# Performance work log

Hardware: AMD Instinct MI355X
Metric: run time of the kernel (lower is better)

Reference implementation:

```python
import jax, jax.numpy as jnp
import numpy as np
from jax import lax

STD_H, STD_W = 364, 280
RADIUS, SIGMA = 15, 4.0


def gaussian_kernel():
    r = jnp.arange(-RADIUS, RADIUS + 1, dtype=jnp.float32)
    d2 = r[:, None] ** 2 + r[None, :] ** 2
    k = jnp.exp(-0.5 / (SIGMA ** 2) * d2)
    k = k / k.sum()
    return k[None, None]  # (1,1,31,31) OIHW


def setup_inputs() -> dict:
    key = jax.random.key(0)
    k1, k2 = jax.random.split(key)
    B, H, W = 32, 512, 512
    input_face = jax.random.uniform(k1, (B, 3, H, W), dtype=jnp.float32)
    # landmarks in (x, y) pixel coords within the HxW image
    landmarks = jax.random.uniform(k2, (B, 68, 2), dtype=jnp.float32) * jnp.array([W, H], jnp.float32)
    weight = gaussian_kernel()
    return {"input_face": input_face, "landmarks": landmarks, "weight": weight}


def _blur(x, weight):
    # x: (B,1,h,w), 31x31 'same' conv (kernel symmetric, so corr == conv)
    return lax.conv_general_dilated(x, weight, (1, 1), 'SAME',
                                    dimension_numbers=('NCHW', 'OIHW', 'NCHW'))


def reference(input_face, landmarks, weight):
    B, C, H, W = input_face.shape
    scaling = STD_H / H
    lm = landmarks * scaling                      # (B,68,2) in standard coords
    center = lm[:, 30:31, :]                      # (B,1,2)

    p0 = lm[:, 30:36, :]
    p1 = lm[:, 2:15, :]
    p2 = lm[:, 48:68, :]
    p3 = lm[:, 6:11, :]
    p01 = (p0 - center) * 1.5 + center
    p11 = (p1 - center) * 0.5 + center
    p12 = (p1 - center) * 0.7 + center
    p13 = (p1 - center) * 0.9 + center
    p21 = (p2 - center) * 1.3 + center
    keys = jnp.concatenate([p0, p01, p12, p13, p11, p2, p3, p21], axis=-2)  # (B,96,2)

    iy = jnp.round(jnp.clip(keys[..., 1], 0, STD_H - 1)).astype(jnp.int32)
    ix = jnp.round(jnp.clip(keys[..., 0], 0, STD_W - 1)).astype(jnp.int32)

    # Faithful to torch advanced-indexing semantics: union of ALL batches'
    # points is written into every batch's heatmap.
    hm = jnp.zeros((STD_H, STD_W), jnp.float32).at[iy.ravel(), ix.ravel()].set(1.0)
    hm = jnp.broadcast_to(hm[None, None], (B, 1, STD_H, STD_W))

    w1 = _blur(hm, weight)
    w2 = jnp.where(w1 > 1e-7, 1.0, w1)
    w3 = _blur(w2, weight)

    w_mask = jax.image.resize(w3, (B, 1, H, W), method='bilinear')
    return (1.0 - w_mask) * input_face  # filling='black'
```

## Files before the change

### kernel.cpp

```cpp
#include <hip/hip_runtime.h>

#define BB   32
#define HH   512
#define WW   512
#define SH   364
#define SW   280
#define RAD  15
#define NK   96
#define OMN  (HH*WW)
#define PF4  (OMN/4)

#define OH   16
#define OW   32
#define NRM  13
#define NCM  19
#define WRM  (NRM + 2*RAD)
#define HRM  (NRM + 4*RAD)
#define HCP  84
#define WCP  52
#define NCP  20
#define G1   13
#define G2   5

typedef float f4 __attribute__((ext_vector_type(4)));

__device__ __forceinline__ void point_ij(const float* __restrict__ lm, int b, int j,
                                         int& ix, int& iy) {
    int idx; float s;
    if      (j <  6) { idx = 30 + j;        s = 1.0f; }
    else if (j < 12) { idx = 30 + (j - 6);  s = 1.5f; }
    else if (j < 25) { idx =  2 + (j - 12); s = 0.7f; }
    else if (j < 38) { idx =  2 + (j - 25); s = 0.9f; }
    else if (j < 51) { idx =  2 + (j - 38); s = 0.5f; }
    else if (j < 71) { idx = 48 + (j - 51); s = 1.0f; }
    else if (j < 76) { idx =  6 + (j - 71); s = 1.0f; }
    else             { idx = 48 + (j - 76); s = 1.3f; }
    const float scal = 364.0f / 512.0f;
    float lx = lm[b * 136 + idx * 2 + 0] * scal;
    float ly = lm[b * 136 + idx * 2 + 1] * scal;
    float kx, ky;
    if (s == 1.0f) { kx = lx; ky = ly; }
    else {
        float cx = lm[b * 136 + 30 * 2 + 0] * scal;
        float cy = lm[b * 136 + 30 * 2 + 1] * scal;
        kx = (lx - cx) * s + cx;
        ky = (ly - cy) * s + cy;
    }
    ix = __float2int_rn(fminf(fmaxf(kx, 0.0f), (float)(SW - 1)));
    iy = __float2int_rn(fminf(fmaxf(ky, 0.0f), (float)(SH - 1)));
}

__global__ __launch_bounds__(256) void k_fused(const float* __restrict__ lm,
                                               const float* __restrict__ wt,
                                               const f4* __restrict__ face,
                                               f4* __restrict__ out) {
    __shared__ float gwl[31];
    __shared__ alignas(16) float hmS[HRM][HCP];
    __shared__ alignas(16) float t1 [HRM][WCP];
    __shared__ alignas(16) float w2S[WRM][WCP];
    __shared__ alignas(16) float t2 [WRM][NCP];
    __shared__ alignas(16) float w3S[NRM][NCP];
    __shared__ alignas(16) float maskS[OH][OW];

    const int tid = threadIdx.x;
    const int h0 = blockIdx.y * OH, w0 = blockIdx.x * OW;
    const float sy = (float)SH / (float)HH;
    const float sx = (float)SW / (float)WW;

    if (tid < 31) gwl[tid] = wt[15 * 31 + tid] / sqrtf(wt[15 * 31 + 15]);

    const int hl = h0 + OH - 1, wl = w0 + OW - 1;
    float fy0 = fmaxf(((float)h0 + 0.5f) * sy - 0.5f, 0.0f);
    float fyl = fminf(((float)hl + 0.5f) * sy - 0.5f, (float)(SH - 1));
    int rbase = (int)fy0;
    int rend  = min(SH - 1, (int)fyl + 1);
    float fx0 = fmaxf(((float)w0 + 0.5f) * sx - 0.5f, 0.0f);
    float fxl = fminf(((float)wl + 0.5f) * sx - 0.5f, (float)(SW - 1));
    int cbase = (int)fx0;
    int cend  = min(SW - 1, (int)fxl + 1);
    int NR = rend - rbase + 1;
    int NC = cend - cbase + 1;
    int HR = NR + 4 * RAD, HC = NC + 4 * RAD;

    for (int i = tid; i < HRM * HCP; i += 256) ((float*)hmS)[i] = 0.0f;
    __syncthreads();

    float g[31];
    #pragma unroll
    for (int k = 0; k < 31; ++k) g[k] = gwl[k];

    for (int p = tid; p < BB * NK; p += 256) {
        int b = p / NK, j = p - b * NK;
        int ix, iy;
        point_ij(lm, b, j, ix, iy);
        int ly = iy - (rbase - 2 * RAD), lx = ix - (cbase - 2 * RAD);
        if (ly >= 0 && ly < HR && lx >= 0 && lx < HC) hmS[ly][lx] = 1.0f;
    }
    __syncthreads();

    for (int it = tid; it < HRM * G1; it += 256) {
        int y = it / G1, c0 = (it - y * G1) * 4;
        float r[34];
        #pragma unroll
        for (int k = 0; k < 34; ++k) r[k] = hmS[y][c0 + k];
        #pragma unroll
        for (int q = 0; q < 4; ++q) {
            float acc = 0.0f;
            #pragma unroll
            for (int d = 0; d < 31; ++d) acc += g[d] * r[q + d];
            t1[y][c0 + q] = acc;
        }
    }
    __syncthreads();

    for (int it = tid; it < WRM * G1; it += 256) {
        int y = it / G1, c0 = (it - y * G1) * 4;
        f4 acc = {0.0f, 0.0f, 0.0f, 0.0f};
        #pragma unroll
        for (int d = 0; d < 31; ++d) {
            f4 v = *(const f4*)&t1[y + d][c0];
            acc += v * g[d];
        }
        int gy = rbase - RAD + y;
        bool rowok = (gy >= 0 && gy < SH);
        #pragma unroll
        for (int q = 0; q < 4; ++q) {
            float v = acc[q];
            v = (v > 1e-7f) ? 1.0f : v;
            int gx = cbase - RAD + c0 + q;
            w2S[y][c0 + q] = (rowok && gx >= 0 && gx < SW) ? v : 0.0f;
        }
    }
    __syncthreads();

    for (int it = tid; it < WRM * G2; it += 256) {
        int y = it / G2, c0 = (it - y * G2) * 4;
        float r[34];
        #pragma unroll
        for (int k = 0; k < 34; ++k) r[k] = w2S[y][c0 + k];
        #pragma unroll
        for (int q = 0; q < 4; ++q) {
            float acc = 0.0f;
            #pragma unroll
            for (int d = 0; d < 31; ++d) acc += g[d] * r[q + d];
            t2[y][c0 + q] = acc;
        }
    }
    __syncthreads();

    for (int it = tid; it < NRM * G2; it += 256) {
        int y = it / G2, c0 = (it - y * G2) * 4;
        f4 acc = {0.0f, 0.0f, 0.0f, 0.0f};
        #pragma unroll
        for (int d = 0; d < 31; ++d) {
            f4 v = *(const f4*)&t2[y + d][c0];
            acc += v * g[d];
        }
        *(f4*)&w3S[y][c0] = acc;
    }
    __syncthreads();

    for (int i = tid; i < OH * OW; i += 256) {
        int dh = i / OW, dw = i - dh * OW;
        int h = h0 + dh, w = w0 + dw;
        float fy = fminf(fmaxf(((float)h + 0.5f) * sy - 0.5f, 0.0f), (float)(SH - 1));
        float fx = fminf(fmaxf(((float)w + 0.5f) * sx - 0.5f, 0.0f), (float)(SW - 1));
        int y0 = (int)fy, x0 = (int)fx;
        int y1 = min(y0 + 1, SH - 1), x1 = min(x0 + 1, SW - 1);
        float ty = fy - (float)y0, tx = fx - (float)x0;
        int ly0 = y0 - rbase, ly1 = y1 - rbase;
        int lx0 = x0 - cbase, lx1 = x1 - cbase;
        float v00 = w3S[ly0][lx0], v01 = w3S[ly0][lx1];
        float v10 = w3S[ly1][lx0], v11 = w3S[ly1][lx1];
        float v = (1.0f - ty) * ((1.0f - tx) * v00 + tx * v01)
                +         ty  * ((1.0f - tx) * v10 + tx * v11);
        maskS[dh][dw] = 1.0f - v;
    }
    __syncthreads();

    const int j   = tid & 127;
    const int grp = tid >> 7;
    const int dh  = j >> 3, dw4 = (j & 7) << 2;
    const f4 m = *(const f4*)&maskS[dh][dw4];
    const long off = (long)(h0 + dh) * (WW / 4) + ((w0 + dw4) >> 2);
    #pragma unroll 8
    for (int k = 0; k < 48; ++k) {
        long idx = (long)(grp + 2 * k) * PF4 + off;
        f4 a = face[idx];
        __builtin_nontemporal_store(a * m, &out[idx]);
    }
}

extern "C" void kernel_launch(void* const* d_in, const int* in_sizes, int n_in,
                              void* d_out, int out_size, void* d_ws, size_t ws_size,
                              hipStream_t stream) {
    const float* face = (const float*)d_in[0];
    const float* lm   = (const float*)d_in[1];
    const float* wt   = (const float*)d_in[2];

    k_fused<<<dim3(WW / OW, HH / OH), 256, 0, stream>>>(
        lm, wt, (const f4*)face, (f4*)d_out);
}
```

Before: 51.78 us.

## Prefetch face tiles before blur stages and vectorize LDS row accesses

Issues 16 global loads of the face image per thread before the blur computation so their latency overlaps the shared-memory convolution stages, then consumes them after the mask is ready. The horizontal blur passes now read shared memory with float4 loads and write results as float4 stores. It also requests two blocks per SM via launch bounds. The prefetch holds 64 extra registers per thread across the blur stages, which with the launch-bounds cap may cause spills or reduce occupancy.

```diff
diff --git a/kernel.cpp b/kernel.cpp
--- a/kernel.cpp
+++ b/kernel.cpp
@@ -50,10 +50,10 @@
     iy = __float2int_rn(fminf(fmaxf(ky, 0.0f), (float)(SH - 1)));
 }
 
-__global__ __launch_bounds__(256) void k_fused(const float* __restrict__ lm,
-                                               const float* __restrict__ wt,
-                                               const f4* __restrict__ face,
-                                               f4* __restrict__ out) {
+__global__ __launch_bounds__(256, 2) void k_fused(const float* __restrict__ lm,
+                                                  const float* __restrict__ wt,
+                                                  const f4* __restrict__ face,
+                                                  f4* __restrict__ out) {
     __shared__ float gwl[31];
     __shared__ alignas(16) float hmS[HRM][HCP];
     __shared__ alignas(16) float t1 [HRM][WCP];
@@ -66,6 +66,11 @@
     const int h0 = blockIdx.y * OH, w0 = blockIdx.x * OW;
     const float sy = (float)SH / (float)HH;
     const float sx = (float)SW / (float)WW;
+
+    const int j   = tid & 127;
+    const int grp = tid >> 7;
+    const int dh  = j >> 3, dw4 = (j & 7) << 2;
+    const long off = (long)(h0 + dh) * (WW / 4) + ((w0 + dw4) >> 2);
 
     if (tid < 31) gwl[tid] = wt[15 * 31 + tid] / sqrtf(wt[15 * 31 + 15]);
 
@@ -90,26 +95,52 @@
     for (int k = 0; k < 31; ++k) g[k] = gwl[k];
 
     for (int p = tid; p < BB * NK; p += 256) {
-        int b = p / NK, j = p - b * NK;
+        int b = p / NK, jj = p - b * NK;
         int ix, iy;
-        point_ij(lm, b, j, ix, iy);
+        point_ij(lm, b, jj, ix, iy);
         int ly = iy - (rbase - 2 * RAD), lx = ix - (cbase - 2 * RAD);
         if (ly >= 0 && ly < HR && lx >= 0 && lx < HC) hmS[ly][lx] = 1.0f;
     }
+
+    f4 pf0  = face[(long)(grp +  0) * PF4 + off];
+    f4 pf1  = face[(long)(grp +  2) * PF4 + off];
+    f4 pf2  = face[(long)(grp +  4) * PF4 + off];
+    f4 pf3  = face[(long)(grp +  6) * PF4 + off];
+    f4 pf4  = face[(long)(grp +  8) * PF4 + off];
+    f4 pf5  = face[(long)(grp + 10) * PF4 + off];
+    f4 pf6  = face[(long)(grp + 12) * PF4 + off];
+    f4 pf7  = face[(long)(grp + 14) * PF4 + off];
+    f4 pf8  = face[(long)(grp + 16) * PF4 + off];
+    f4 pf9  = face[(long)(grp + 18) * PF4 + off];
+    f4 pf10 = face[(long)(grp + 20) * PF4 + off];
+    f4 pf11 = face[(long)(grp + 22) * PF4 + off];
+    f4 pf12 = face[(long)(grp + 24) * PF4 + off];
+    f4 pf13 = face[(long)(grp + 26) * PF4 + off];
+    f4 pf14 = face[(long)(grp + 28) * PF4 + off];
+    f4 pf15 = face[(long)(grp + 30) * PF4 + off];
+
     __syncthreads();
 
     for (int it = tid; it < HRM * G1; it += 256) {
-        int y = it / G1, c0 = (it - y * G1) * 4;
-        float r[34];
-        #pragma unroll
-        for (int k = 0; k < 34; ++k) r[k] = hmS[y][c0 + k];
+        int y = it / G1, c0g = it - y * G1;
+        f4 rb[9];
+        #pragma unroll
+        for (int k = 0; k < 9; ++k) rb[k] = *(const f4*)&hmS[y][(c0g + k) * 4];
+        float r[36];
+        #pragma unroll
+        for (int k = 0; k < 9; ++k) {
+            r[4*k+0] = rb[k][0]; r[4*k+1] = rb[k][1];
+            r[4*k+2] = rb[k][2]; r[4*k+3] = rb[k][3];
+        }
+        f4 o;
         #pragma unroll
         for (int q = 0; q < 4; ++q) {
             float acc = 0.0f;
             #pragma unroll
             for (int d = 0; d < 31; ++d) acc += g[d] * r[q + d];
-            t1[y][c0 + q] = acc;
-        }
+            o[q] = acc;
+        }
+        *(f4*)&t1[y][c0g * 4] = o;
     }
     __syncthreads();
 
@@ -123,28 +154,38 @@
         }
         int gy = rbase - RAD + y;
         bool rowok = (gy >= 0 && gy < SH);
+        f4 o;
         #pragma unroll
         for (int q = 0; q < 4; ++q) {
             float v = acc[q];
             v = (v > 1e-7f) ? 1.0f : v;
             int gx = cbase - RAD + c0 + q;
-            w2S[y][c0 + q] = (rowok && gx >= 0 && gx < SW) ? v : 0.0f;
-        }
+            o[q] = (rowok && gx >= 0 && gx < SW) ? v : 0.0f;
+        }
+        *(f4*)&w2S[y][c0] = o;
     }
     __syncthreads();
 
     for (int it = tid; it < WRM * G2; it += 256) {
-        int y = it / G2, c0 = (it - y * G2) * 4;
-        float r[34];
-        #pragma unroll
-        for (int k = 0; k < 34; ++k) r[k] = w2S[y][c0 + k];
+        int y = it / G2, c0g = it - y * G2;
+        f4 rb[9];
+        #pragma unroll
+        for (int k = 0; k < 9; ++k) rb[k] = *(const f4*)&w2S[y][(c0g + k) * 4];
+        float r[36];
+        #pragma unroll
+        for (int k = 0; k < 9; ++k) {
+            r[4*k+0] = rb[k][0]; r[4*k+1] = rb[k][1];
+            r[4*k+2] = rb[k][2]; r[4*k+3] = rb[k][3];
+        }
+        f4 o;
         #pragma unroll
         for (int q = 0; q < 4; ++q) {
             float acc = 0.0f;
             #pragma unroll
             for (int d = 0; d < 31; ++d) acc += g[d] * r[q + d];
-            t2[y][c0 + q] = acc;
-        }
+            o[q] = acc;
+        }
+        *(f4*)&t2[y][c0g * 4] = o;
     }
     __syncthreads();
 
@@ -161,8 +202,8 @@
     __syncthreads();
 
     for (int i = tid; i < OH * OW; i += 256) {
-        int dh = i / OW, dw = i - dh * OW;
-        int h = h0 + dh, w = w0 + dw;
+        int ddh = i / OW, ddw = i - ddh * OW;
+        int h = h0 + ddh, w = w0 + ddw;
         float fy = fminf(fmaxf(((float)h + 0.5f) * sy - 0.5f, 0.0f), (float)(SH - 1));
         float fx = fminf(fmaxf(((float)w + 0.5f) * sx - 0.5f, 0.0f), (float)(SW - 1));
         int y0 = (int)fy, x0 = (int)fx;
@@ -174,17 +215,29 @@
         float v10 = w3S[ly1][lx0], v11 = w3S[ly1][lx1];
         float v = (1.0f - ty) * ((1.0f - tx) * v00 + tx * v01)
                 +         ty  * ((1.0f - tx) * v10 + tx * v11);
-        maskS[dh][dw] = 1.0f - v;
-    }
-    __syncthreads();
-
-    const int j   = tid & 127;
-    const int grp = tid >> 7;
-    const int dh  = j >> 3, dw4 = (j & 7) << 2;
+        maskS[ddh][ddw] = 1.0f - v;
+    }
+    __syncthreads();
+
     const f4 m = *(const f4*)&maskS[dh][dw4];
-    const long off = (long)(h0 + dh) * (WW / 4) + ((w0 + dw4) >> 2);
+    __builtin_nontemporal_store(pf0  * m, &out[(long)(grp +  0) * PF4 + off]);
+    __builtin_nontemporal_store(pf1  * m, &out[(long)(grp +  2) * PF4 + off]);
+    __builtin_nontemporal_store(pf2  * m, &out[(long)(grp +  4) * PF4 + off]);
+    __builtin_nontemporal_store(pf3  * m, &out[(long)(grp +  6) * PF4 + off]);
+    __builtin_nontemporal_store(pf4  * m, &out[(long)(grp +  8) * PF4 + off]);
+    __builtin_nontemporal_store(pf5  * m, &out[(long)(grp + 10) * PF4 + off]);
+    __builtin_nontemporal_store(pf6  * m, &out[(long)(grp + 12) * PF4 + off]);
+    __builtin_nontemporal_store(pf7  * m, &out[(long)(grp + 14) * PF4 + off]);
+    __builtin_nontemporal_store(pf8  * m, &out[(long)(grp + 16) * PF4 + off]);
+    __builtin_nontemporal_store(pf9  * m, &out[(long)(grp + 18) * PF4 + off]);
+    __builtin_nontemporal_store(pf10 * m, &out[(long)(grp + 20) * PF4 + off]);
+    __builtin_nontemporal_store(pf11 * m, &out[(long)(grp + 22) * PF4 + off]);
+    __builtin_nontemporal_store(pf12 * m, &out[(long)(grp + 24) * PF4 + off]);
+    __builtin_nontemporal_store(pf13 * m, &out[(long)(grp + 26) * PF4 + off]);
+    __builtin_nontemporal_store(pf14 * m, &out[(long)(grp + 28) * PF4 + off]);
+    __builtin_nontemporal_store(pf15 * m, &out[(long)(grp + 30) * PF4 + off]);
     #pragma unroll 8
-    for (int k = 0; k < 48; ++k) {
+    for (int k = 16; k < 48; ++k) {
         long idx = (long)(grp + 2 * k) * PF4 + off;
         f4 a = face[idx];
         __builtin_nontemporal_store(a * m, &out[idx]);
```

After: 50.98 us (median of 2 runs). No clear change (-1.5%).
